# Optimization experiments

Hardware: AMD Instinct MI355X
Metric: run time of the kernel (lower is better)

Reference implementation:

```python
import jax, jax.numpy as jnp
import numpy as np

B, T, K, H = 256, 2048, 64, 256
NUM_PRED = 512


def setup_inputs() -> dict:
    key = jax.random.key(0)
    ks = jax.random.split(key, 13)
    s = 0.05
    G = 4 * H
    return {
        "input": jax.random.normal(ks[0], (B, T), jnp.float32),
        "conv_w": jax.random.normal(ks[1], (K,), jnp.float32) * s,
        "conv_b": jax.random.normal(ks[2], (K,), jnp.float32) * s,
        "W_ih0": jax.random.normal(ks[3], (G, K), jnp.float32) * s,
        "W_hh0": jax.random.normal(ks[4], (G, H), jnp.float32) * s,
        "b_ih0": jax.random.normal(ks[5], (G,), jnp.float32) * s,
        "b_hh0": jax.random.normal(ks[6], (G,), jnp.float32) * s,
        "W_ih1": jax.random.normal(ks[7], (G, H), jnp.float32) * s,
        "W_hh1": jax.random.normal(ks[8], (G, H), jnp.float32) * s,
        "b_ih1": jax.random.normal(ks[9], (G,), jnp.float32) * s,
        "b_hh1": jax.random.normal(ks[10], (G,), jnp.float32) * s,
        "lin_w": jax.random.normal(ks[11], (1, H), jnp.float32) * s,
        "lin_b": jax.random.normal(ks[12], (1,), jnp.float32) * s,
        "num_predictions": NUM_PRED,
    }


def _cell(x, h, c, Wi, Wh, bi, bh):
    # PyTorch LSTM cell: gate order i, f, g, o
    g = x @ Wi.T + h @ Wh.T + bi + bh
    i, f, gg, o = jnp.split(g, 4, axis=-1)
    i = jax.nn.sigmoid(i)
    f = jax.nn.sigmoid(f)
    gg = jnp.tanh(gg)
    o = jax.nn.sigmoid(o)
    c_new = f * c + i * gg
    h_new = o * jnp.tanh(c_new)
    return h_new, c_new


def reference(input, conv_w, conv_b, W_ih0, W_hh0, b_ih0, b_hh0,
              W_ih1, W_hh1, b_ih1, b_hh1, lin_w, lin_b, num_predictions):
    Bn, Tn = input.shape
    Kn = conv_w.shape[0]
    Hh = W_hh0.shape[1]

    # cnn: [B,1,T] -> Conv1d(1,K,1) -> [B,K,T] -> ReLU -> torch.reshape to (B,T,K)
    # NOTE: original uses reshape (not transpose); replicate faithfully.
    c_raw = jax.nn.relu(input[:, None, :] * conv_w[None, :, None] + conv_b[None, :, None])  # [B,K,T]
    c_out = c_raw.reshape(Bn, Tn, Kn)  # faithful reshape-as-in-source

    def step(carry, x):
        h0, c0, h1, c1 = carry
        h0, c0 = _cell(x, h0, c0, W_ih0, W_hh0, b_ih0, b_hh0)
        h1, c1 = _cell(h0, h1, c1, W_ih1, W_hh1, b_ih1, b_hh1)
        return (h0, c0, h1, c1), None

    z = jnp.zeros((Bn, Hh), input.dtype)
    carry, _ = jax.lax.scan(step, (z, z, z, z), jnp.swapaxes(c_out, 0, 1))  # scan over T
    pred0 = carry[2] @ lin_w.T + lin_b  # [B,1], output of last warmup step

    def ar_step(carry, _):
        h0, c0, h1, c1, last = carry
        x = jax.nn.relu(last[:, None] * conv_w[None, :] + conv_b[None, :])  # [B,K]
        h0, c0 = _cell(x, h0, c0, W_ih0, W_hh0, b_ih0, b_hh0)
        h1, c1 = _cell(h0, h1, c1, W_ih1, W_hh1, b_ih1, b_hh1)
        p = (h1 @ lin_w.T + lin_b)[:, 0]  # [B]
        return (h0, c0, h1, c1, p), p

    init = (*carry, pred0[:, 0])
    _, preds = jax.lax.scan(ar_step, init, None, length=num_predictions - 1)  # [P-1, B]
    return jnp.concatenate([pred0, preds.T], axis=1)  # [B, num_predictions]
```

## Files before the change

### kernel.cpp

```cpp
#include <hip/hip_runtime.h>
#include <hip/hip_bf16.h>
#include <cstdint>

#define TT 2048
#define NPRED 512
#define NSTEP (TT + NPRED)

typedef _Float16 f16;
typedef __attribute__((ext_vector_type(8))) _Float16 f16x8;
typedef __attribute__((ext_vector_type(4))) float f32x4;

#define WB0_OFF   0u
#define WB1_OFF   655360u
#define BIAS0_OFF 1703936u
#define BIAS1_OFF 1708032u
#define HX0_OFF   1712128u
#define HX1_OFF   1974272u
#define FLAG_OFF  2236416u
#define PACC_OFF  2244608u

static __device__ __forceinline__ float sigmoidf_(float x) {
    return 1.0f / (1.0f + __expf(-x));
}

static __device__ __forceinline__ uint2 ld8u(const unsigned short* p) {
    unsigned long long v = __hip_atomic_load((const unsigned long long*)p,
                                             __ATOMIC_RELAXED, __HIP_MEMORY_SCOPE_AGENT);
    uint2 r; r.x = (unsigned)v; r.y = (unsigned)(v >> 32); return r;
}
static __device__ __forceinline__ float ld1a(const float* p) {
    unsigned v = __hip_atomic_load((const unsigned*)p,
                                   __ATOMIC_RELAXED, __HIP_MEMORY_SCOPE_AGENT);
    return __uint_as_float(v);
}
static __device__ __forceinline__ void st1a(float* p, float v) {
    __hip_atomic_store((unsigned*)p, __float_as_uint(v),
                       __ATOMIC_RELAXED, __HIP_MEMORY_SCOPE_AGENT);
}
static __device__ __forceinline__ void st4a(unsigned* p, unsigned v) {
    __hip_atomic_store(p, v, __ATOMIC_RELAXED, __HIP_MEMORY_SCOPE_AGENT);
}
static __device__ __forceinline__ unsigned short f16bits(float x) {
    union { f16 h; unsigned short u; } cv;
    cv.h = (f16)x;
    return cv.u;
}

#define N0_ELEM 327680
#define N1_ELEM 524288

__global__ __launch_bounds__(256) void prep_kernel(
    const float* __restrict__ W_ih0, const float* __restrict__ W_hh0,
    const float* __restrict__ b_ih0, const float* __restrict__ b_hh0,
    const float* __restrict__ W_ih1, const float* __restrict__ W_hh1,
    const float* __restrict__ b_ih1, const float* __restrict__ b_hh1,
    f16* __restrict__ WB0, f16* __restrict__ WB1,
    float* __restrict__ bias0P, float* __restrict__ bias1P,
    unsigned int* __restrict__ flags, float* __restrict__ p_part)
{
    int idx = blockIdx.x * 256 + threadIdx.x;
    if (idx < N0_ELEM) {
        int e = idx & 7, l = (idx >> 3) & 63;
        int rest = idx >> 9;
        int fr = rest % 10, sw = rest / 10;
        int w = sw & 3, slice = sw >> 2;
        int q = l & 3, jj = (l & 15) >> 2;
        int row = q * 256 + slice * 16 + 4 * w + jj;
        int k = fr * 32 + (l >> 4) * 8 + e;
        float v = (k < 64) ? W_ih0[row * 64 + k] : W_hh0[row * 256 + (k - 64)];
        WB0[idx] = (f16)v;
    } else if (idx < N0_ELEM + N1_ELEM) {
        int i2 = idx - N0_ELEM;
        int e = i2 & 7, l = (i2 >> 3) & 63;
        int rest = i2 >> 9;
        int fr = rest & 15, sw = rest >> 4;
        int w = sw & 3, slice = sw >> 2;
        int q = l & 3, jj = (l & 15) >> 2;
        int row = q * 256 + slice * 16 + 4 * w + jj;
        int k = fr * 32 + (l >> 4) * 8 + e;
        float v = (k < 256) ? W_ih1[row * 256 + k] : W_hh1[row * 256 + (k - 256)];
        WB1[i2] = (f16)v;
    } else if (idx < N0_ELEM + N1_ELEM + 1024) {
        int r = idx - (N0_ELEM + N1_ELEM);
        int j = r >> 2, q = r & 3;
        bias0P[r] = b_ih0[q * 256 + j] + b_hh0[q * 256 + j];
    } else if (idx < N0_ELEM + N1_ELEM + 2048) {
        int r = idx - (N0_ELEM + N1_ELEM + 1024);
        int j = r >> 2, q = r & 3;
        bias1P[r] = b_ih1[q * 256 + j] + b_hh1[q * 256 + j];
    } else if (idx < N0_ELEM + N1_ELEM + 2048 + 2048) {
        flags[idx - (N0_ELEM + N1_ELEM + 2048)] = 0u;
    } else if (idx < N0_ELEM + N1_ELEM + 2048 + 2048 + 8192) {
        p_part[idx - (N0_ELEM + N1_ELEM + 2048 + 2048)] = 0.f;
    }
}

__global__ __launch_bounds__(256) void fused_kernel(
    const float* __restrict__ input,
    const float* __restrict__ conv_w, const float* __restrict__ conv_b,
    const f16* __restrict__ WB0, const f16* __restrict__ WB1,
    const float* __restrict__ bias0P, const float* __restrict__ bias1P,
    const float* __restrict__ lin_w, const float* __restrict__ lin_b,
    unsigned short* hx0, unsigned short* hx1,
    unsigned int* flags, float* p_part,
    float* __restrict__ out)
{
    const int t = threadIdx.x;
    const int lane = t & 63, w = t >> 6;
    const int g = blockIdx.x & 15, slice = blockIdx.x >> 4;

    __shared__ __align__(16) f16 Ah[18 * 65 * 8];
    __shared__ __align__(16) float gbuf0[16 * 68 + 4];
    __shared__ __align__(16) float gbuf1[16 * 68 + 4];
    __shared__ float cw_s[64], cb_s[64], lw_s[256];
    __shared__ float p_lds[16];

    f16x8 B0[10], B1[16];
    {
        const f16* p0 = WB0 + ((size_t)(slice * 4 + w) * 10 * 64 + lane) * 8;
        #pragma unroll
        for (int f = 0; f < 10; ++f) B0[f] = *(const f16x8*)(p0 + f * 512);
        const f16* p1 = WB1 + ((size_t)(slice * 4 + w) * 16 * 64 + lane) * 8;
        #pragma unroll
        for (int f = 0; f < 16; ++f) B1[f] = *(const f16x8*)(p1 + f * 512);
    }

    if (t < 64) { cw_s[t] = conv_w[t]; cb_s[t] = conv_b[t]; }
    lw_s[t] = lin_w[t];

    #pragma unroll
    for (int i = 0; i < 4; ++i) {
        int c = t + 256 * i;
        int d = ((2 + (c >> 6)) * 65 + (c & 63)) * 8;
        f16x8 z = {};
        *(f16x8*)(Ah + d) = z;
    }

    const int ub = t >> 4, uj = t & 15;
    const int jg = slice * 16 + uj;
    const float4 bs0 = *(const float4*)(bias0P + 4 * jg);
    const float4 bs1 = *(const float4*)(bias1P + 4 * jg);
    float c0 = 0.f, c1 = 0.f;
    const float linb = lin_b[0];

    const int rb = t & 15;
    const int rest = t >> 4;
    const int bg0 = g * 16;

    unsigned int* fl0 = flags + (size_t)g * 64;
    unsigned int* cnp = flags + (size_t)(16 + g) * 64;

    __syncthreads();

    #pragma unroll 1
    for (int k = 0; k < TT; ++k) {
        if (k >= 1) {
            const unsigned short* s0 = hx0 + (size_t)((k - 1) & 1) * 65536 + (size_t)(bg0 + rb) * 256;
            #pragma unroll
            for (int it = 0; it < 2; ++it) {
                int oct = rest + 16 * it;
                uint2 a = ld8u(s0 + oct * 8);
                uint2 b = ld8u(s0 + oct * 8 + 4);
                int d = ((2 + (oct >> 2)) * 65 + (rb + 16 * (oct & 3))) * 8;
                *(uint4*)(Ah + d) = make_uint4(a.x, a.y, b.x, b.y);
            }
        }
        if (k >= 2) {
            const unsigned short* s1 = hx1 + (size_t)((k - 1) & 1) * 65536 + (size_t)(bg0 + rb) * 256;
            #pragma unroll
            for (int it = 0; it < 2; ++it) {
                int oct = rest + 16 * it;
                uint2 a = ld8u(s1 + oct * 8);
                uint2 b = ld8u(s1 + oct * 8 + 4);
                int d = ((10 + (oct >> 2)) * 65 + (rb + 16 * (oct & 3))) * 8;
                *(uint4*)(Ah + d) = make_uint4(a.x, a.y, b.x, b.y);
            }
        }
        if (t < 128) {
            int rb2 = t & 15, xoct = t >> 4;
            int k0 = xoct * 8;
            const float* inprow = input + (size_t)(bg0 + rb2) * TT + ((k & 31) << 6);
            float cwv = cw_s[k >> 5], cbv = cb_s[k >> 5];
            f16x8 hv;
            #pragma unroll
            for (int e = 0; e < 8; ++e)
                hv[e] = (f16)fmaxf(inprow[k0 + e] * cwv + cbv, 0.f);
            int d = ((xoct >> 2) * 65 + (rb2 + 16 * (xoct & 3))) * 8;
            *(f16x8*)(Ah + d) = hv;
        }
        __syncthreads();

        {
            f32x4 acc = {0.f, 0.f, 0.f, 0.f};
            #pragma unroll
            for (int f = 0; f < 10; ++f) {
                f16x8 a = *(const f16x8*)(Ah + (f * 65 + lane) * 8);
                acc = __builtin_amdgcn_mfma_f32_16x16x32_f16(a, B0[f], acc, 0, 0, 0);
            }
            int rr = w * 16 + (lane & 15);
            int bb = (lane >> 4) * 4;
            #pragma unroll
            for (int qq = 0; qq < 4; ++qq) gbuf0[(bb + qq) * 68 + rr] = acc[qq];
        }
        if (k >= 1) {
            f32x4 acc = {0.f, 0.f, 0.f, 0.f};
            #pragma unroll
            for (int f = 0; f < 16; ++f) {
                f16x8 a = *(const f16x8*)(Ah + ((2 + f) * 65 + lane) * 8);
                acc = __builtin_amdgcn_mfma_f32_16x16x32_f16(a, B1[f], acc, 0, 0, 0);
            }
            int rr = w * 16 + (lane & 15);
            int bb = (lane >> 4) * 4;
            #pragma unroll
            for (int qq = 0; qq < 4; ++qq) gbuf1[(bb + qq) * 68 + rr] = acc[qq];
        }
        __syncthreads();

        {
            float4 gv = *(const float4*)(gbuf0 + ub * 68 + uj * 4);
            float gi = gv.x + bs0.x, gf = gv.y + bs0.y, gg = gv.z + bs0.z, go = gv.w + bs0.w;
            float cn = sigmoidf_(gf) * c0 + sigmoidf_(gi) * tanhf(gg);
            float hn = sigmoidf_(go) * tanhf(cn);
            c0 = cn;
            unsigned short hb = f16bits(hn);
            int oth = __shfl_xor((int)hb, 1);
            if (!(uj & 1)) {
                unsigned word = (unsigned)hb | ((unsigned)(oth & 0xffff) << 16);
                st4a((unsigned*)(hx0 + (size_t)(k & 1) * 65536 + (size_t)(bg0 + ub) * 256 + jg), word);
            }
        }
        if (k >= 1) {
            float4 gv = *(const float4*)(gbuf1 + ub * 68 + uj * 4);
            float gi = gv.x + bs1.x, gf = gv.y + bs1.y, gg = gv.z + bs1.z, go = gv.w + bs1.w;
            float cn = sigmoidf_(gf) * c1 + sigmoidf_(gi) * tanhf(gg);
            float hn = sigmoidf_(go) * tanhf(cn);
            c1 = cn;
            unsigned short hb = f16bits(hn);
            int oth = __shfl_xor((int)hb, 1);
            if (!(uj & 1)) {
                unsigned word = (unsigned)hb | ((unsigned)(oth & 0xffff) << 16);
                st4a((unsigned*)(hx1 + (size_t)(k & 1) * 65536 + (size_t)(bg0 + ub) * 256 + jg), word);
            }
        }
        __syncthreads();
        if (t == 0) {
            __hip_atomic_fetch_add(fl0, 1u, __ATOMIC_RELAXED, __HIP_MEMORY_SCOPE_AGENT);
            unsigned tgt = 16u * (unsigned)(k + 1);
            while (__hip_atomic_load(fl0, __ATOMIC_RELAXED, __HIP_MEMORY_SCOPE_AGENT) < tgt)
                __builtin_amdgcn_s_sleep(1);
        }
        __syncthreads();
    }

    #pragma unroll 1
    for (int k = TT; k < NSTEP; ++k) {
        {
            const unsigned short* s0 = hx0 + (size_t)((k - 1) & 1) * 65536 + (size_t)(bg0 + rb) * 256;
            const unsigned short* s1 = hx1 + (size_t)((k - 1) & 1) * 65536 + (size_t)(bg0 + rb) * 256;
            #pragma unroll
            for (int it = 0; it < 2; ++it) {
                int oct = rest + 16 * it;
                uint2 a0 = ld8u(s0 + oct * 8);
                uint2 b0 = ld8u(s0 + oct * 8 + 4);
                int d = ((2 + (oct >> 2)) * 65 + (rb + 16 * (oct & 3))) * 8;
                *(uint4*)(Ah + d) = make_uint4(a0.x, a0.y, b0.x, b0.y);
                uint2 a1 = ld8u(s1 + oct * 8);
                uint2 b1 = ld8u(s1 + oct * 8 + 4);
                d = ((10 + (oct >> 2)) * 65 + (rb + 16 * (oct & 3))) * 8;
                *(uint4*)(Ah + d) = make_uint4(a1.x, a1.y, b1.x, b1.y);
            }
        }
        __syncthreads();

        {
            f32x4 acc = {0.f, 0.f, 0.f, 0.f};
            #pragma unroll
            for (int f = 0; f < 16; ++f) {
                f16x8 a = *(const f16x8*)(Ah + ((2 + f) * 65 + lane) * 8);
                acc = __builtin_amdgcn_mfma_f32_16x16x32_f16(a, B1[f], acc, 0, 0, 0);
            }
            int rr = w * 16 + (lane & 15);
            int bb = (lane >> 4) * 4;
            #pragma unroll
            for (int qq = 0; qq < 4; ++qq) gbuf1[(bb + qq) * 68 + rr] = acc[qq];
        }
        __syncthreads();

        {
            float4 gv = *(const float4*)(gbuf1 + ub * 68 + uj * 4);
            float gi = gv.x + bs1.x, gf = gv.y + bs1.y, gg = gv.z + bs1.z, go = gv.w + bs1.w;
            float cn = sigmoidf_(gf) * c1 + sigmoidf_(gi) * tanhf(gg);
            float hn = sigmoidf_(go) * tanhf(cn);
            c1 = cn;
            unsigned short hb = f16bits(hn);
            int oth = __shfl_xor((int)hb, 1);
            if (!(uj & 1)) {
                unsigned word = (unsigned)hb | ((unsigned)(oth & 0xffff) << 16);
                st4a((unsigned*)(hx1 + (size_t)(k & 1) * 65536 + (size_t)(bg0 + ub) * 256 + jg), word);
            }
            float pp = hn * lw_s[jg];
            pp += __shfl_xor(pp, 1);
            pp += __shfl_xor(pp, 2);
            pp += __shfl_xor(pp, 4);
            pp += __shfl_xor(pp, 8);
            if (uj == 0)
                st1a(p_part + (size_t)(k & 1) * 4096 + (size_t)slice * 256 + (bg0 + ub), pp);
        }
        __syncthreads();
        if (t == 0) {
            __hip_atomic_fetch_add(cnp, 1u, __ATOMIC_RELAXED, __HIP_MEMORY_SCOPE_AGENT);
            unsigned tgt = 16u * (unsigned)(k - TT + 1);
            while (__hip_atomic_load(cnp, __ATOMIC_RELAXED, __HIP_MEMORY_SCOPE_AGENT) < tgt)
                __builtin_amdgcn_s_sleep(1);
        }
        __syncthreads();

        if (t < 16) {
            const float* pb = p_part + (size_t)(k & 1) * 4096;
            float ps = 0.f;
            #pragma unroll
            for (int sl = 0; sl < 16; ++sl) ps += ld1a(pb + sl * 256 + bg0 + t);
            float p = ps + linb;
            p_lds[t] = p;
            if (slice == 0) out[(size_t)(bg0 + t) * NPRED + (k - TT)] = p;
        }
        if (k == NSTEP - 1) break;
        __syncthreads();

        if (t < 128) {
            int rb2 = t & 15, xoct = t >> 4;
            int k0 = xoct * 8;
            float p = p_lds[rb2];
            f16x8 hv;
            #pragma unroll
            for (int e = 0; e < 8; ++e)
                hv[e] = (f16)fmaxf(p * cw_s[k0 + e] + cb_s[k0 + e], 0.f);
            int d = ((xoct >> 2) * 65 + (rb2 + 16 * (xoct & 3))) * 8;
            *(f16x8*)(Ah + d) = hv;
        }
        __syncthreads();

        {
            f32x4 acc = {0.f, 0.f, 0.f, 0.f};
            #pragma unroll
            for (int f = 0; f < 10; ++f) {
                f16x8 a = *(const f16x8*)(Ah + (f * 65 + lane) * 8);
                acc = __builtin_amdgcn_mfma_f32_16x16x32_f16(a, B0[f], acc, 0, 0, 0);
            }
            int rr = w * 16 + (lane & 15);
            int bb = (lane >> 4) * 4;
            #pragma unroll
            for (int qq = 0; qq < 4; ++qq) gbuf0[(bb + qq) * 68 + rr] = acc[qq];
        }
        __syncthreads();
        {
            float4 gv = *(const float4*)(gbuf0 + ub * 68 + uj * 4);
            float gi = gv.x + bs0.x, gf = gv.y + bs0.y, gg = gv.z + bs0.z, go = gv.w + bs0.w;
            float cn = sigmoidf_(gf) * c0 + sigmoidf_(gi) * tanhf(gg);
            float hn = sigmoidf_(go) * tanhf(cn);
            c0 = cn;
            unsigned short hb = f16bits(hn);
            int oth = __shfl_xor((int)hb, 1);
            if (!(uj & 1)) {
                unsigned word = (unsigned)hb | ((unsigned)(oth & 0xffff) << 16);
                st4a((unsigned*)(hx0 + (size_t)(k & 1) * 65536 + (size_t)(bg0 + ub) * 256 + jg), word);
            }
        }
        __syncthreads();
        if (t == 0) {
            __hip_atomic_fetch_add(fl0, 1u, __ATOMIC_RELAXED, __HIP_MEMORY_SCOPE_AGENT);
            unsigned tgt = 16u * (unsigned)(k + 1);
            while (__hip_atomic_load(fl0, __ATOMIC_RELAXED, __HIP_MEMORY_SCOPE_AGENT) < tgt)
                __builtin_amdgcn_s_sleep(1);
        }
        __syncthreads();
    }
}

extern "C" void kernel_launch(void* const* d_in, const int* in_sizes, int n_in,
                              void* d_out, int out_size, void* d_ws, size_t ws_size,
                              hipStream_t stream) {
    const float* input  = (const float*)d_in[0];
    const float* conv_w = (const float*)d_in[1];
    const float* conv_b = (const float*)d_in[2];
    const float* W_ih0  = (const float*)d_in[3];
    const float* W_hh0  = (const float*)d_in[4];
    const float* b_ih0  = (const float*)d_in[5];
    const float* b_hh0  = (const float*)d_in[6];
    const float* W_ih1  = (const float*)d_in[7];
    const float* W_hh1  = (const float*)d_in[8];
    const float* b_ih1  = (const float*)d_in[9];
    const float* b_hh1  = (const float*)d_in[10];
    const float* lin_w  = (const float*)d_in[11];
    const float* lin_b  = (const float*)d_in[12];
    float* out = (float*)d_out;

    uint8_t* ws = (uint8_t*)d_ws;
    f16* WB0 = (f16*)(ws + WB0_OFF);
    f16* WB1 = (f16*)(ws + WB1_OFF);
    float* bias0P = (float*)(ws + BIAS0_OFF);
    float* bias1P = (float*)(ws + BIAS1_OFF);
    unsigned short* hx0 = (unsigned short*)(ws + HX0_OFF);
    unsigned short* hx1 = (unsigned short*)(ws + HX1_OFF);
    unsigned int* flags = (unsigned int*)(ws + FLAG_OFF);
    float* p_part = (float*)(ws + PACC_OFF);

    prep_kernel<<<3376, 256, 0, stream>>>(W_ih0, W_hh0, b_ih0, b_hh0,
                                          W_ih1, W_hh1, b_ih1, b_hh1,
                                          WB0, WB1, bias0P, bias1P, flags, p_part);

    fused_kernel<<<256, 256, 0, stream>>>(input, conv_w, conv_b,
                                          WB0, WB1, bias0P, bias1P,
                                          lin_w, lin_b, hx0, hx1, flags, p_part, out);
}
```

Baseline: 9.296 ms.

## Replace per-step counter barriers with step-tagged 64-bit hidden-state words

```diff
diff --git a/kernel.cpp b/kernel.cpp
--- a/kernel.cpp
+++ b/kernel.cpp
@@ -9,35 +9,23 @@
 typedef _Float16 f16;
 typedef __attribute__((ext_vector_type(8))) _Float16 f16x8;
 typedef __attribute__((ext_vector_type(4))) float f32x4;
+typedef unsigned long long u64;
 
 #define WB0_OFF   0u
 #define WB1_OFF   655360u
 #define BIAS0_OFF 1703936u
 #define BIAS1_OFF 1708032u
 #define HX0_OFF   1712128u
-#define HX1_OFF   1974272u
-#define FLAG_OFF  2236416u
-#define PACC_OFF  2244608u
+#define HX1_OFF   2498560u
+#define PPW_OFF   3284992u
 
 static __device__ __forceinline__ float sigmoidf_(float x) {
     return 1.0f / (1.0f + __expf(-x));
 }
-
-static __device__ __forceinline__ uint2 ld8u(const unsigned short* p) {
-    unsigned long long v = __hip_atomic_load((const unsigned long long*)p,
-                                             __ATOMIC_RELAXED, __HIP_MEMORY_SCOPE_AGENT);
-    uint2 r; r.x = (unsigned)v; r.y = (unsigned)(v >> 32); return r;
-}
-static __device__ __forceinline__ float ld1a(const float* p) {
-    unsigned v = __hip_atomic_load((const unsigned*)p,
-                                   __ATOMIC_RELAXED, __HIP_MEMORY_SCOPE_AGENT);
-    return __uint_as_float(v);
-}
-static __device__ __forceinline__ void st1a(float* p, float v) {
-    __hip_atomic_store((unsigned*)p, __float_as_uint(v),
-                       __ATOMIC_RELAXED, __HIP_MEMORY_SCOPE_AGENT);
-}
-static __device__ __forceinline__ void st4a(unsigned* p, unsigned v) {
+static __device__ __forceinline__ u64 lda8(const u64* p) {
+    return __hip_atomic_load(p, __ATOMIC_RELAXED, __HIP_MEMORY_SCOPE_AGENT);
+}
+static __device__ __forceinline__ void sta8(u64* p, u64 v) {
     __hip_atomic_store(p, v, __ATOMIC_RELAXED, __HIP_MEMORY_SCOPE_AGENT);
 }
 static __device__ __forceinline__ unsigned short f16bits(float x) {
@@ -48,6 +36,9 @@
 
 #define N0_ELEM 327680
 #define N1_ELEM 524288
+#define WBASE   (N0_ELEM + N1_ELEM + 2048)
+#define HXW_CNT (3 * 256 * 128)
+#define PPW_CNT (2 * 16 * 256)
 
 __global__ __launch_bounds__(256) void prep_kernel(
     const float* __restrict__ W_ih0, const float* __restrict__ W_hh0,
@@ -56,7 +47,7 @@
     const float* __restrict__ b_ih1, const float* __restrict__ b_hh1,
     f16* __restrict__ WB0, f16* __restrict__ WB1,
     float* __restrict__ bias0P, float* __restrict__ bias1P,
-    unsigned int* __restrict__ flags, float* __restrict__ p_part)
+    u64* __restrict__ hx0w, u64* __restrict__ hx1w, u64* __restrict__ ppw)
 {
     int idx = blockIdx.x * 256 + threadIdx.x;
     if (idx < N0_ELEM) {
@@ -88,10 +79,12 @@
         int r = idx - (N0_ELEM + N1_ELEM + 1024);
         int j = r >> 2, q = r & 3;
         bias1P[r] = b_ih1[q * 256 + j] + b_hh1[q * 256 + j];
-    } else if (idx < N0_ELEM + N1_ELEM + 2048 + 2048) {
-        flags[idx - (N0_ELEM + N1_ELEM + 2048)] = 0u;
-    } else if (idx < N0_ELEM + N1_ELEM + 2048 + 2048 + 8192) {
-        p_part[idx - (N0_ELEM + N1_ELEM + 2048 + 2048)] = 0.f;
+    } else if (idx < WBASE + 2 * HXW_CNT) {
+        int r = idx - WBASE;
+        if (r < HXW_CNT) hx0w[r] = ~0ull;
+        else             hx1w[r - HXW_CNT] = ~0ull;
+    } else if (idx < WBASE + 2 * HXW_CNT + PPW_CNT) {
+        ppw[idx - (WBASE + 2 * HXW_CNT)] = ~0ull;
     }
 }
 
@@ -101,8 +94,7 @@
     const f16* __restrict__ WB0, const f16* __restrict__ WB1,
     const float* __restrict__ bias0P, const float* __restrict__ bias1P,
     const float* __restrict__ lin_w, const float* __restrict__ lin_b,
-    unsigned short* hx0, unsigned short* hx1,
-    unsigned int* flags, float* p_part,
+    u64* hx0w, u64* hx1w, u64* ppw,
     float* __restrict__ out)
 {
     const int t = threadIdx.x;
@@ -147,35 +139,10 @@
     const int rest = t >> 4;
     const int bg0 = g * 16;
 
-    unsigned int* fl0 = flags + (size_t)g * 64;
-    unsigned int* cnp = flags + (size_t)(16 + g) * 64;
-
     __syncthreads();
 
     #pragma unroll 1
     for (int k = 0; k < TT; ++k) {
-        if (k >= 1) {
-            const unsigned short* s0 = hx0 + (size_t)((k - 1) & 1) * 65536 + (size_t)(bg0 + rb) * 256;
-            #pragma unroll
-            for (int it = 0; it < 2; ++it) {
-                int oct = rest + 16 * it;
-                uint2 a = ld8u(s0 + oct * 8);
-                uint2 b = ld8u(s0 + oct * 8 + 4);
-                int d = ((2 + (oct >> 2)) * 65 + (rb + 16 * (oct & 3))) * 8;
-                *(uint4*)(Ah + d) = make_uint4(a.x, a.y, b.x, b.y);
-            }
-        }
-        if (k >= 2) {
-            const unsigned short* s1 = hx1 + (size_t)((k - 1) & 1) * 65536 + (size_t)(bg0 + rb) * 256;
-            #pragma unroll
-            for (int it = 0; it < 2; ++it) {
-                int oct = rest + 16 * it;
-                uint2 a = ld8u(s1 + oct * 8);
-                uint2 b = ld8u(s1 + oct * 8 + 4);
-                int d = ((10 + (oct >> 2)) * 65 + (rb + 16 * (oct & 3))) * 8;
-                *(uint4*)(Ah + d) = make_uint4(a.x, a.y, b.x, b.y);
-            }
-        }
         if (t < 128) {
             int rb2 = t & 15, xoct = t >> 4;
             int k0 = xoct * 8;
@@ -187,6 +154,58 @@
                 hv[e] = (f16)fmaxf(inprow[k0 + e] * cwv + cbv, 0.f);
             int d = ((xoct >> 2) * 65 + (rb2 + 16 * (xoct & 3))) * 8;
             *(f16x8*)(Ah + d) = hv;
+        }
+        if (k >= 1) {
+            const u64* s0 = hx0w + (size_t)((k - 1) % 3) * 32768 + (size_t)(bg0 + rb) * 128;
+            const u64* s1 = hx1w + (size_t)((k >= 2 ? (k - 2) % 3 : 0)) * 32768 + (size_t)(bg0 + rb) * 128;
+            const unsigned tag0 = (unsigned)(k - 1), tag1 = (unsigned)(k - 2);
+            const bool need1 = (k >= 2);
+            u64 v[16];
+            #pragma unroll
+            for (int i = 0; i < 4; ++i) v[i]      = lda8(s0 + rest * 4 + i);
+            #pragma unroll
+            for (int i = 0; i < 4; ++i) v[4 + i]  = lda8(s0 + (rest + 16) * 4 + i);
+            if (need1) {
+                #pragma unroll
+                for (int i = 0; i < 4; ++i) v[8 + i]  = lda8(s1 + rest * 4 + i);
+                #pragma unroll
+                for (int i = 0; i < 4; ++i) v[12 + i] = lda8(s1 + (rest + 16) * 4 + i);
+            }
+            for (;;) {
+                bool ok = true;
+                #pragma unroll
+                for (int i = 0; i < 8; ++i) ok &= ((unsigned)(v[i] >> 32) == tag0);
+                if (need1) {
+                    #pragma unroll
+                    for (int i = 8; i < 16; ++i) ok &= ((unsigned)(v[i] >> 32) == tag1);
+                }
+                if (ok) break;
+                __builtin_amdgcn_s_sleep(1);
+                #pragma unroll
+                for (int i = 0; i < 4; ++i) if ((unsigned)(v[i] >> 32) != tag0) v[i] = lda8(s0 + rest * 4 + i);
+                #pragma unroll
+                for (int i = 0; i < 4; ++i) if ((unsigned)(v[4+i] >> 32) != tag0) v[4+i] = lda8(s0 + (rest + 16) * 4 + i);
+                if (need1) {
+                    #pragma unroll
+                    for (int i = 0; i < 4; ++i) if ((unsigned)(v[8+i] >> 32) != tag1) v[8+i] = lda8(s1 + rest * 4 + i);
+                    #pragma unroll
+                    for (int i = 0; i < 4; ++i) if ((unsigned)(v[12+i] >> 32) != tag1) v[12+i] = lda8(s1 + (rest + 16) * 4 + i);
+                }
+            }
+            int oct = rest;
+            *(uint4*)(Ah + ((2 + (oct >> 2)) * 65 + (rb + 16 * (oct & 3))) * 8) =
+                make_uint4((unsigned)v[0], (unsigned)v[1], (unsigned)v[2], (unsigned)v[3]);
+            oct = rest + 16;
+            *(uint4*)(Ah + ((2 + (oct >> 2)) * 65 + (rb + 16 * (oct & 3))) * 8) =
+                make_uint4((unsigned)v[4], (unsigned)v[5], (unsigned)v[6], (unsigned)v[7]);
+            if (need1) {
+                oct = rest;
+                *(uint4*)(Ah + ((10 + (oct >> 2)) * 65 + (rb + 16 * (oct & 3))) * 8) =
+                    make_uint4((unsigned)v[8], (unsigned)v[9], (unsigned)v[10], (unsigned)v[11]);
+                oct = rest + 16;
+                *(uint4*)(Ah + ((10 + (oct >> 2)) * 65 + (rb + 16 * (oct & 3))) * 8) =
+                    make_uint4((unsigned)v[12], (unsigned)v[13], (unsigned)v[14], (unsigned)v[15]);
+            }
         }
         __syncthreads();
 
@@ -225,8 +244,9 @@
             unsigned short hb = f16bits(hn);
             int oth = __shfl_xor((int)hb, 1);
             if (!(uj & 1)) {
-                unsigned word = (unsigned)hb | ((unsigned)(oth & 0xffff) << 16);
-                st4a((unsigned*)(hx0 + (size_t)(k & 1) * 65536 + (size_t)(bg0 + ub) * 256 + jg), word);
+                unsigned lo = (unsigned)hb | ((unsigned)(oth & 0xffff) << 16);
+                sta8(hx0w + (size_t)(k % 3) * 32768 + (size_t)(bg0 + ub) * 128 + (jg >> 1),
+                     ((u64)(unsigned)k << 32) | lo);
             }
         }
         if (k >= 1) {
@@ -238,37 +258,55 @@
             unsigned short hb = f16bits(hn);
             int oth = __shfl_xor((int)hb, 1);
             if (!(uj & 1)) {
-                unsigned word = (unsigned)hb | ((unsigned)(oth & 0xffff) << 16);
-                st4a((unsigned*)(hx1 + (size_t)(k & 1) * 65536 + (size_t)(bg0 + ub) * 256 + jg), word);
-            }
-        }
-        __syncthreads();
-        if (t == 0) {
-            __hip_atomic_fetch_add(fl0, 1u, __ATOMIC_RELAXED, __HIP_MEMORY_SCOPE_AGENT);
-            unsigned tgt = 16u * (unsigned)(k + 1);
-            while (__hip_atomic_load(fl0, __ATOMIC_RELAXED, __HIP_MEMORY_SCOPE_AGENT) < tgt)
-                __builtin_amdgcn_s_sleep(1);
-        }
-        __syncthreads();
+                unsigned lo = (unsigned)hb | ((unsigned)(oth & 0xffff) << 16);
+                sta8(hx1w + (size_t)((k - 1) % 3) * 32768 + (size_t)(bg0 + ub) * 128 + (jg >> 1),
+                     ((u64)(unsigned)(k - 1) << 32) | lo);
+            }
+        }
     }
 
     #pragma unroll 1
     for (int k = TT; k < NSTEP; ++k) {
         {
-            const unsigned short* s0 = hx0 + (size_t)((k - 1) & 1) * 65536 + (size_t)(bg0 + rb) * 256;
-            const unsigned short* s1 = hx1 + (size_t)((k - 1) & 1) * 65536 + (size_t)(bg0 + rb) * 256;
-            #pragma unroll
-            for (int it = 0; it < 2; ++it) {
-                int oct = rest + 16 * it;
-                uint2 a0 = ld8u(s0 + oct * 8);
-                uint2 b0 = ld8u(s0 + oct * 8 + 4);
-                int d = ((2 + (oct >> 2)) * 65 + (rb + 16 * (oct & 3))) * 8;
-                *(uint4*)(Ah + d) = make_uint4(a0.x, a0.y, b0.x, b0.y);
-                uint2 a1 = ld8u(s1 + oct * 8);
-                uint2 b1 = ld8u(s1 + oct * 8 + 4);
-                d = ((10 + (oct >> 2)) * 65 + (rb + 16 * (oct & 3))) * 8;
-                *(uint4*)(Ah + d) = make_uint4(a1.x, a1.y, b1.x, b1.y);
-            }
+            const u64* s0 = hx0w + (size_t)((k - 1) % 3) * 32768 + (size_t)(bg0 + rb) * 128;
+            const u64* s1 = hx1w + (size_t)((k - 2) % 3) * 32768 + (size_t)(bg0 + rb) * 128;
+            const unsigned tag0 = (unsigned)(k - 1), tag1 = (unsigned)(k - 2);
+            u64 v[16];
+            #pragma unroll
+            for (int i = 0; i < 4; ++i) v[i]      = lda8(s0 + rest * 4 + i);
+            #pragma unroll
+            for (int i = 0; i < 4; ++i) v[4 + i]  = lda8(s0 + (rest + 16) * 4 + i);
+            #pragma unroll
+            for (int i = 0; i < 4; ++i) v[8 + i]  = lda8(s1 + rest * 4 + i);
+            #pragma unroll
+            for (int i = 0; i < 4; ++i) v[12 + i] = lda8(s1 + (rest + 16) * 4 + i);
+            for (;;) {
+                bool ok = true;
+                #pragma unroll
+                for (int i = 0; i < 8; ++i) ok &= ((unsigned)(v[i] >> 32) == tag0);
+                #pragma unroll
+                for (int i = 8; i < 16; ++i) ok &= ((unsigned)(v[i] >> 32) == tag1);
+                if (ok) break;
+                __builtin_amdgcn_s_sleep(1);
+                #pragma unroll
+                for (int i = 0; i < 4; ++i) if ((unsigned)(v[i] >> 32) != tag0) v[i] = lda8(s0 + rest * 4 + i);
+                #pragma unroll
+                for (int i = 0; i < 4; ++i) if ((unsigned)(v[4+i] >> 32) != tag0) v[4+i] = lda8(s0 + (rest + 16) * 4 + i);
+                #pragma unroll
+                for (int i = 0; i < 4; ++i) if ((unsigned)(v[8+i] >> 32) != tag1) v[8+i] = lda8(s1 + rest * 4 + i);
+                #pragma unroll
+                for (int i = 0; i < 4; ++i) if ((unsigned)(v[12+i] >> 32) != tag1) v[12+i] = lda8(s1 + (rest + 16) * 4 + i);
+            }
+            int oct = rest;
+            *(uint4*)(Ah + ((2 + (oct >> 2)) * 65 + (rb + 16 * (oct & 3))) * 8) =
+                make_uint4((unsigned)v[0], (unsigned)v[1], (unsigned)v[2], (unsigned)v[3]);
+            *(uint4*)(Ah + ((10 + (oct >> 2)) * 65 + (rb + 16 * (oct & 3))) * 8) =
+                make_uint4((unsigned)v[8], (unsigned)v[9], (unsigned)v[10], (unsigned)v[11]);
+            oct = rest + 16;
+            *(uint4*)(Ah + ((2 + (oct >> 2)) * 65 + (rb + 16 * (oct & 3))) * 8) =
+                make_uint4((unsigned)v[4], (unsigned)v[5], (unsigned)v[6], (unsigned)v[7]);
+            *(uint4*)(Ah + ((10 + (oct >> 2)) * 65 + (rb + 16 * (oct & 3))) * 8) =
+                make_uint4((unsigned)v[12], (unsigned)v[13], (unsigned)v[14], (unsigned)v[15]);
         }
         __syncthreads();
 
@@ -295,8 +333,9 @@
             unsigned short hb = f16bits(hn);
             int oth = __shfl_xor((int)hb, 1);
             if (!(uj & 1)) {
-                unsigned word = (unsigned)hb | ((unsigned)(oth & 0xffff) << 16);
-                st4a((unsigned*)(hx1 + (size_t)(k & 1) * 65536 + (size_t)(bg0 + ub) * 256 + jg), word);
+                unsigned lo = (unsigned)hb | ((unsigned)(oth & 0xffff) << 16);
+                sta8(hx1w + (size_t)((k - 1) % 3) * 32768 + (size_t)(bg0 + ub) * 128 + (jg >> 1),
+                     ((u64)(unsigned)(k - 1) << 32) | lo);
             }
             float pp = hn * lw_s[jg];
             pp += __shfl_xor(pp, 1);
@@ -304,28 +343,34 @@
             pp += __shfl_xor(pp, 4);
             pp += __shfl_xor(pp, 8);
             if (uj == 0)
-                st1a(p_part + (size_t)(k & 1) * 4096 + (size_t)slice * 256 + (bg0 + ub), pp);
-        }
-        __syncthreads();
-        if (t == 0) {
-            __hip_atomic_fetch_add(cnp, 1u, __ATOMIC_RELAXED, __HIP_MEMORY_SCOPE_AGENT);
-            unsigned tgt = 16u * (unsigned)(k - TT + 1);
-            while (__hip_atomic_load(cnp, __ATOMIC_RELAXED, __HIP_MEMORY_SCOPE_AGENT) < tgt)
+                sta8(ppw + (size_t)(k & 1) * 4096 + (size_t)slice * 256 + (bg0 + ub),
+                     ((u64)(unsigned)k << 32) | (u64)__float_as_uint(pp));
+        }
+
+        if (t < 16) {
+            const u64* pb = ppw + (size_t)(k & 1) * 4096;
+            u64 pv[16];
+            #pragma unroll
+            for (int sl = 0; sl < 16; ++sl) pv[sl] = lda8(pb + sl * 256 + bg0 + t);
+            for (;;) {
+                bool ok = true;
+                #pragma unroll
+                for (int sl = 0; sl < 16; ++sl) ok &= ((unsigned)(pv[sl] >> 32) == (unsigned)k);
+                if (ok) break;
                 __builtin_amdgcn_s_sleep(1);
-        }
-        __syncthreads();
-
-        if (t < 16) {
-            const float* pb = p_part + (size_t)(k & 1) * 4096;
+                #pragma unroll
+                for (int sl = 0; sl < 16; ++sl)
+                    if ((unsigned)(pv[sl] >> 32) != (unsigned)k) pv[sl] = lda8(pb + sl * 256 + bg0 + t);
+            }
             float ps = 0.f;
             #pragma unroll
-            for (int sl = 0; sl < 16; ++sl) ps += ld1a(pb + sl * 256 + bg0 + t);
+            for (int sl = 0; sl < 16; ++sl) ps += __uint_as_float((unsigned)pv[sl]);
             float p = ps + linb;
             p_lds[t] = p;
             if (slice == 0) out[(size_t)(bg0 + t) * NPRED + (k - TT)] = p;
         }
+        __syncthreads();
         if (k == NSTEP - 1) break;
-        __syncthreads();
 
         if (t < 128) {
             int rb2 = t & 15, xoct = t >> 4;
@@ -362,18 +407,11 @@
             unsigned short hb = f16bits(hn);
             int oth = __shfl_xor((int)hb, 1);
             if (!(uj & 1)) {
-                unsigned word = (unsigned)hb | ((unsigned)(oth & 0xffff) << 16);
-                st4a((unsigned*)(hx0 + (size_t)(k & 1) * 65536 + (size_t)(bg0 + ub) * 256 + jg), word);
-            }
-        }
-        __syncthreads();
-        if (t == 0) {
-            __hip_atomic_fetch_add(fl0, 1u, __ATOMIC_RELAXED, __HIP_MEMORY_SCOPE_AGENT);
-            unsigned tgt = 16u * (unsigned)(k + 1);
-            while (__hip_atomic_load(fl0, __ATOMIC_RELAXED, __HIP_MEMORY_SCOPE_AGENT) < tgt)
-                __builtin_amdgcn_s_sleep(1);
-        }
-        __syncthreads();
+                unsigned lo = (unsigned)hb | ((unsigned)(oth & 0xffff) << 16);
+                sta8(hx0w + (size_t)(k % 3) * 32768 + (size_t)(bg0 + ub) * 128 + (jg >> 1),
+                     ((u64)(unsigned)k << 32) | lo);
+            }
+        }
     }
 }
 
@@ -400,16 +438,16 @@
     f16* WB1 = (f16*)(ws + WB1_OFF);
     float* bias0P = (float*)(ws + BIAS0_OFF);
     float* bias1P = (float*)(ws + BIAS1_OFF);
-    unsigned short* hx0 = (unsigned short*)(ws + HX0_OFF);
-    unsigned short* hx1 = (unsigned short*)(ws + HX1_OFF);
-    unsigned int* flags = (unsigned int*)(ws + FLAG_OFF);
-    float* p_part = (float*)(ws + PACC_OFF);
-
-    prep_kernel<<<3376, 256, 0, stream>>>(W_ih0, W_hh0, b_ih0, b_hh0,
+    u64* hx0w = (u64*)(ws + HX0_OFF);
+    u64* hx1w = (u64*)(ws + HX1_OFF);
+    u64* ppw  = (u64*)(ws + PPW_OFF);
+
+    prep_kernel<<<4136, 256, 0, stream>>>(W_ih0, W_hh0, b_ih0, b_hh0,
                                           W_ih1, W_hh1, b_ih1, b_hh1,
-                                          WB0, WB1, bias0P, bias1P, flags, p_part);
+                                          WB0, WB1, bias0P, bias1P,
+                                          hx0w, hx1w, ppw);
 
     fused_kernel<<<256, 256, 0, stream>>>(input, conv_w, conv_b,
                                           WB0, WB1, bias0P, bias1P,
-                                          lin_w, lin_b, hx0, hx1, flags, p_part, out);
-}
+                                          lin_w, lin_b, hx0w, hx1w, ppw, out);
+}
```

Result: slower. 11.91 ms (+28.1%).

## Apply LSTM gates in MFMA registers via lane shuffles, signal flags per wave

Applied to the files above, without the earlier changes.

```diff
diff --git a/kernel.cpp b/kernel.cpp
--- a/kernel.cpp
+++ b/kernel.cpp
@@ -44,6 +44,13 @@
     union { f16 h; unsigned short u; } cv;
     cv.h = (f16)x;
     return cv.u;
+}
+
+static __device__ __forceinline__ void xpose4(int lane, float& v0, float& v1, float& v2, float& v3) {
+    { float x = (lane & 1) ? v0 : v1; x = __shfl_xor(x, 1); if (lane & 1) v0 = x; else v1 = x; }
+    { float x = (lane & 1) ? v2 : v3; x = __shfl_xor(x, 1); if (lane & 1) v2 = x; else v3 = x; }
+    { float x = (lane & 2) ? v0 : v2; x = __shfl_xor(x, 2); if (lane & 2) v0 = x; else v2 = x; }
+    { float x = (lane & 2) ? v1 : v3; x = __shfl_xor(x, 2); if (lane & 2) v1 = x; else v3 = x; }
 }
 
 #define N0_ELEM 327680
@@ -110,10 +117,9 @@
     const int g = blockIdx.x & 15, slice = blockIdx.x >> 4;
 
     __shared__ __align__(16) f16 Ah[18 * 65 * 8];
-    __shared__ __align__(16) float gbuf0[16 * 68 + 4];
-    __shared__ __align__(16) float gbuf1[16 * 68 + 4];
-    __shared__ float cw_s[64], cb_s[64], lw_s[256];
+    __shared__ float cw_s[64], cb_s[64];
     __shared__ float p_lds[16];
+    __shared__ float p_part4[4][16];
 
     f16x8 B0[10], B1[16];
     {
@@ -126,7 +132,6 @@
     }
 
     if (t < 64) { cw_s[t] = conv_w[t]; cb_s[t] = conv_b[t]; }
-    lw_s[t] = lin_w[t];
 
     #pragma unroll
     for (int i = 0; i < 4; ++i) {
@@ -136,10 +141,12 @@
         *(f16x8*)(Ah + d) = z;
     }
 
-    const int ub = t >> 4, uj = t & 15;
-    const int jg = slice * 16 + uj;
-    const float4 bs0 = *(const float4*)(bias0P + 4 * jg);
-    const float4 bs1 = *(const float4*)(bias1P + 4 * jg);
+    const int ujl = w * 4 + ((lane & 15) >> 2);
+    const int jgl = slice * 16 + ujl;
+    const int Bl  = (lane >> 4) * 4 + (lane & 3);
+    const float4 bs0l = *(const float4*)(bias0P + 4 * jgl);
+    const float4 bs1l = *(const float4*)(bias1P + 4 * jgl);
+    const float lwl = lin_w[jgl];
     float c0 = 0.f, c1 = 0.f;
     const float linb = lin_b[0];
 
@@ -190,62 +197,53 @@
         }
         __syncthreads();
 
-        {
-            f32x4 acc = {0.f, 0.f, 0.f, 0.f};
-            #pragma unroll
-            for (int f = 0; f < 10; ++f) {
-                f16x8 a = *(const f16x8*)(Ah + (f * 65 + lane) * 8);
-                acc = __builtin_amdgcn_mfma_f32_16x16x32_f16(a, B0[f], acc, 0, 0, 0);
-            }
-            int rr = w * 16 + (lane & 15);
-            int bb = (lane >> 4) * 4;
-            #pragma unroll
-            for (int qq = 0; qq < 4; ++qq) gbuf0[(bb + qq) * 68 + rr] = acc[qq];
-        }
+        f32x4 a0 = {0.f, 0.f, 0.f, 0.f};
+        #pragma unroll
+        for (int f = 0; f < 10; ++f) {
+            f16x8 a = *(const f16x8*)(Ah + (f * 65 + lane) * 8);
+            a0 = __builtin_amdgcn_mfma_f32_16x16x32_f16(a, B0[f], a0, 0, 0, 0);
+        }
+        f32x4 a1 = {0.f, 0.f, 0.f, 0.f};
         if (k >= 1) {
-            f32x4 acc = {0.f, 0.f, 0.f, 0.f};
             #pragma unroll
             for (int f = 0; f < 16; ++f) {
                 f16x8 a = *(const f16x8*)(Ah + ((2 + f) * 65 + lane) * 8);
-                acc = __builtin_amdgcn_mfma_f32_16x16x32_f16(a, B1[f], acc, 0, 0, 0);
-            }
-            int rr = w * 16 + (lane & 15);
-            int bb = (lane >> 4) * 4;
-            #pragma unroll
-            for (int qq = 0; qq < 4; ++qq) gbuf1[(bb + qq) * 68 + rr] = acc[qq];
-        }
-        __syncthreads();
+                a1 = __builtin_amdgcn_mfma_f32_16x16x32_f16(a, B1[f], a1, 0, 0, 0);
+            }
+        }
 
         {
-            float4 gv = *(const float4*)(gbuf0 + ub * 68 + uj * 4);
-            float gi = gv.x + bs0.x, gf = gv.y + bs0.y, gg = gv.z + bs0.z, go = gv.w + bs0.w;
-            float cn = sigmoidf_(gf) * c0 + sigmoidf_(gi) * tanhf(gg);
-            float hn = sigmoidf_(go) * tanhf(cn);
+            float v0 = a0[0], v1 = a0[1], v2 = a0[2], v3 = a0[3];
+            xpose4(lane, v0, v1, v2, v3);
+            float cn = sigmoidf_(v1 + bs0l.y) * c0 + sigmoidf_(v0 + bs0l.x) * tanhf(v2 + bs0l.z);
+            float hn = sigmoidf_(v3 + bs0l.w) * tanhf(cn);
             c0 = cn;
             unsigned short hb = f16bits(hn);
-            int oth = __shfl_xor((int)hb, 1);
-            if (!(uj & 1)) {
+            int oth = __shfl_xor((int)hb, 4);
+            if (!(lane & 4)) {
                 unsigned word = (unsigned)hb | ((unsigned)(oth & 0xffff) << 16);
-                st4a((unsigned*)(hx0 + (size_t)(k & 1) * 65536 + (size_t)(bg0 + ub) * 256 + jg), word);
+                st4a((unsigned*)(hx0 + (size_t)(k & 1) * 65536 + (size_t)(bg0 + Bl) * 256 + (jgl & ~1)), word);
             }
         }
         if (k >= 1) {
-            float4 gv = *(const float4*)(gbuf1 + ub * 68 + uj * 4);
-            float gi = gv.x + bs1.x, gf = gv.y + bs1.y, gg = gv.z + bs1.z, go = gv.w + bs1.w;
-            float cn = sigmoidf_(gf) * c1 + sigmoidf_(gi) * tanhf(gg);
-            float hn = sigmoidf_(go) * tanhf(cn);
+            float v0 = a1[0], v1 = a1[1], v2 = a1[2], v3 = a1[3];
+            xpose4(lane, v0, v1, v2, v3);
+            float cn = sigmoidf_(v1 + bs1l.y) * c1 + sigmoidf_(v0 + bs1l.x) * tanhf(v2 + bs1l.z);
+            float hn = sigmoidf_(v3 + bs1l.w) * tanhf(cn);
             c1 = cn;
             unsigned short hb = f16bits(hn);
-            int oth = __shfl_xor((int)hb, 1);
-            if (!(uj & 1)) {
+            int oth = __shfl_xor((int)hb, 4);
+            if (!(lane & 4)) {
                 unsigned word = (unsigned)hb | ((unsigned)(oth & 0xffff) << 16);
-                st4a((unsigned*)(hx1 + (size_t)(k & 1) * 65536 + (size_t)(bg0 + ub) * 256 + jg), word);
-            }
-        }
-        __syncthreads();
+                st4a((unsigned*)(hx1 + (size_t)(k & 1) * 65536 + (size_t)(bg0 + Bl) * 256 + (jgl & ~1)), word);
+            }
+        }
+
+        asm volatile("s_waitcnt vmcnt(0)" ::: "memory");
+        if (lane == 0)
+            __hip_atomic_fetch_add(fl0, 1u, __ATOMIC_RELAXED, __HIP_MEMORY_SCOPE_AGENT);
         if (t == 0) {
-            __hip_atomic_fetch_add(fl0, 1u, __ATOMIC_RELAXED, __HIP_MEMORY_SCOPE_AGENT);
-            unsigned tgt = 16u * (unsigned)(k + 1);
+            unsigned tgt = 64u * (unsigned)(k + 1);
             while (__hip_atomic_load(fl0, __ATOMIC_RELAXED, __HIP_MEMORY_SCOPE_AGENT) < tgt)
                 __builtin_amdgcn_s_sleep(1);
         }
@@ -260,51 +258,46 @@
             #pragma unroll
             for (int it = 0; it < 2; ++it) {
                 int oct = rest + 16 * it;
-                uint2 a0 = ld8u(s0 + oct * 8);
-                uint2 b0 = ld8u(s0 + oct * 8 + 4);
+                uint2 a0v = ld8u(s0 + oct * 8);
+                uint2 b0v = ld8u(s0 + oct * 8 + 4);
                 int d = ((2 + (oct >> 2)) * 65 + (rb + 16 * (oct & 3))) * 8;
-                *(uint4*)(Ah + d) = make_uint4(a0.x, a0.y, b0.x, b0.y);
-                uint2 a1 = ld8u(s1 + oct * 8);
-                uint2 b1 = ld8u(s1 + oct * 8 + 4);
+                *(uint4*)(Ah + d) = make_uint4(a0v.x, a0v.y, b0v.x, b0v.y);
+                uint2 a1v = ld8u(s1 + oct * 8);
+                uint2 b1v = ld8u(s1 + oct * 8 + 4);
                 d = ((10 + (oct >> 2)) * 65 + (rb + 16 * (oct & 3))) * 8;
-                *(uint4*)(Ah + d) = make_uint4(a1.x, a1.y, b1.x, b1.y);
+                *(uint4*)(Ah + d) = make_uint4(a1v.x, a1v.y, b1v.x, b1v.y);
             }
         }
         __syncthreads();
 
         {
-            f32x4 acc = {0.f, 0.f, 0.f, 0.f};
+            f32x4 a1 = {0.f, 0.f, 0.f, 0.f};
             #pragma unroll
             for (int f = 0; f < 16; ++f) {
                 f16x8 a = *(const f16x8*)(Ah + ((2 + f) * 65 + lane) * 8);
-                acc = __builtin_amdgcn_mfma_f32_16x16x32_f16(a, B1[f], acc, 0, 0, 0);
-            }
-            int rr = w * 16 + (lane & 15);
-            int bb = (lane >> 4) * 4;
-            #pragma unroll
-            for (int qq = 0; qq < 4; ++qq) gbuf1[(bb + qq) * 68 + rr] = acc[qq];
-        }
-        __syncthreads();
-
-        {
-            float4 gv = *(const float4*)(gbuf1 + ub * 68 + uj * 4);
-            float gi = gv.x + bs1.x, gf = gv.y + bs1.y, gg = gv.z + bs1.z, go = gv.w + bs1.w;
-            float cn = sigmoidf_(gf) * c1 + sigmoidf_(gi) * tanhf(gg);
-            float hn = sigmoidf_(go) * tanhf(cn);
+                a1 = __builtin_amdgcn_mfma_f32_16x16x32_f16(a, B1[f], a1, 0, 0, 0);
+            }
+            float v0 = a1[0], v1 = a1[1], v2 = a1[2], v3 = a1[3];
+            xpose4(lane, v0, v1, v2, v3);
+            float cn = sigmoidf_(v1 + bs1l.y) * c1 + sigmoidf_(v0 + bs1l.x) * tanhf(v2 + bs1l.z);
+            float hn = sigmoidf_(v3 + bs1l.w) * tanhf(cn);
             c1 = cn;
             unsigned short hb = f16bits(hn);
-            int oth = __shfl_xor((int)hb, 1);
-            if (!(uj & 1)) {
+            int oth = __shfl_xor((int)hb, 4);
+            if (!(lane & 4)) {
                 unsigned word = (unsigned)hb | ((unsigned)(oth & 0xffff) << 16);
-                st4a((unsigned*)(hx1 + (size_t)(k & 1) * 65536 + (size_t)(bg0 + ub) * 256 + jg), word);
-            }
-            float pp = hn * lw_s[jg];
-            pp += __shfl_xor(pp, 1);
-            pp += __shfl_xor(pp, 2);
+                st4a((unsigned*)(hx1 + (size_t)(k & 1) * 65536 + (size_t)(bg0 + Bl) * 256 + (jgl & ~1)), word);
+            }
+            float pp = hn * lwl;
             pp += __shfl_xor(pp, 4);
             pp += __shfl_xor(pp, 8);
-            if (uj == 0)
-                st1a(p_part + (size_t)(k & 1) * 4096 + (size_t)slice * 256 + (bg0 + ub), pp);
+            if ((lane & 12) == 0) p_part4[w][Bl] = pp;
+        }
+        __syncthreads();
+
+        if (t < 16) {
+            float s4 = (p_part4[0][t] + p_part4[1][t]) + (p_part4[2][t] + p_part4[3][t]);
+            st1a(p_part + (size_t)(k & 1) * 4096 + (size_t)slice * 256 + (bg0 + t), s4);
         }
         __syncthreads();
         if (t == 0) {
@@ -341,35 +334,29 @@
         __syncthreads();
 
         {
-            f32x4 acc = {0.f, 0.f, 0.f, 0.f};
+            f32x4 a0 = {0.f, 0.f, 0.f, 0.f};
             #pragma unroll
             for (int f = 0; f < 10; ++f) {
                 f16x8 a = *(const f16x8*)(Ah + (f * 65 + lane) * 8);
-                acc = __builtin_amdgcn_mfma_f32_16x16x32_f16(a, B0[f], acc, 0, 0, 0);
-            }
-            int rr = w * 16 + (lane & 15);
-            int bb = (lane >> 4) * 4;
-            #pragma unroll
-            for (int qq = 0; qq < 4; ++qq) gbuf0[(bb + qq) * 68 + rr] = acc[qq];
-        }
-        __syncthreads();
-        {
-            float4 gv = *(const float4*)(gbuf0 + ub * 68 + uj * 4);
-            float gi = gv.x + bs0.x, gf = gv.y + bs0.y, gg = gv.z + bs0.z, go = gv.w + bs0.w;
-            float cn = sigmoidf_(gf) * c0 + sigmoidf_(gi) * tanhf(gg);
-            float hn = sigmoidf_(go) * tanhf(cn);
+                a0 = __builtin_amdgcn_mfma_f32_16x16x32_f16(a, B0[f], a0, 0, 0, 0);
+            }
+            float v0 = a0[0], v1 = a0[1], v2 = a0[2], v3 = a0[3];
+            xpose4(lane, v0, v1, v2, v3);
+            float cn = sigmoidf_(v1 + bs0l.y) * c0 + sigmoidf_(v0 + bs0l.x) * tanhf(v2 + bs0l.z);
+            float hn = sigmoidf_(v3 + bs0l.w) * tanhf(cn);
             c0 = cn;
             unsigned short hb = f16bits(hn);
-            int oth = __shfl_xor((int)hb, 1);
-            if (!(uj & 1)) {
+            int oth = __shfl_xor((int)hb, 4);
+            if (!(lane & 4)) {
                 unsigned word = (unsigned)hb | ((unsigned)(oth & 0xffff) << 16);
-                st4a((unsigned*)(hx0 + (size_t)(k & 1) * 65536 + (size_t)(bg0 + ub) * 256 + jg), word);
-            }
-        }
-        __syncthreads();
+                st4a((unsigned*)(hx0 + (size_t)(k & 1) * 65536 + (size_t)(bg0 + Bl) * 256 + (jgl & ~1)), word);
+            }
+        }
+        asm volatile("s_waitcnt vmcnt(0)" ::: "memory");
+        if (lane == 0)
+            __hip_atomic_fetch_add(fl0, 1u, __ATOMIC_RELAXED, __HIP_MEMORY_SCOPE_AGENT);
         if (t == 0) {
-            __hip_atomic_fetch_add(fl0, 1u, __ATOMIC_RELAXED, __HIP_MEMORY_SCOPE_AGENT);
-            unsigned tgt = 16u * (unsigned)(k + 1);
+            unsigned tgt = 64u * (unsigned)(k + 1);
             while (__hip_atomic_load(fl0, __ATOMIC_RELAXED, __HIP_MEMORY_SCOPE_AGENT) < tgt)
                 __builtin_amdgcn_s_sleep(1);
         }
```

After: 14.89 ms. 1.6x slower.
